# Optimization experiments

Measured on AMD Instinct MI355X. Metric: run time of the kernel, lower is better.

The kernel has to match this reference:

```python
import jax, jax.numpy as jnp
import numpy as np

L = 5          # num_layers
N = 50000      # nodes
E = 600000     # edges
D = 128        # num_features == hidden_units
G = 256        # graphs in batch
O = 10         # num_outputs
BN_EPS = 1e-5


def setup_inputs() -> dict:
    key = jax.random.key(0)
    ks = jax.random.split(key, 8)
    x = jax.random.normal(ks[0], (N, D), jnp.float32)
    edge_index = jax.random.randint(ks[1], (2, E), 0, N, jnp.int32)
    edge_attr = jax.random.randint(ks[2], (E, 3), 0, 8, jnp.int32)
    batch = jnp.sort(jax.random.randint(ks[3], (N,), 0, G, jnp.int32))
    s = 0.05
    return {
        "x": x,
        "edge_index": edge_index,
        "edge_attr": edge_attr,
        "batch": batch,
        "bond_emb": jax.random.normal(ks[4], (L, 3, 8, D), jnp.float32) * s,
        "conv_w1": jax.random.normal(ks[5], (L, D, D), jnp.float32) * s,
        "conv_b1": jnp.zeros((L, D), jnp.float32),
        "conv_bn_gamma": jnp.ones((L, D), jnp.float32),
        "conv_bn_beta": jnp.zeros((L, D), jnp.float32),
        "conv_bn_mean": jnp.zeros((L, D), jnp.float32),
        "conv_bn_var": jnp.ones((L, D), jnp.float32),
        "conv_w2": jax.random.normal(ks[6], (L, D, D), jnp.float32) * s,
        "conv_b2": jnp.zeros((L, D), jnp.float32),
        "bn_gamma": jnp.ones((L, D), jnp.float32),
        "bn_beta": jnp.zeros((L, D), jnp.float32),
        "bn_mean": jnp.zeros((L, D), jnp.float32),
        "bn_var": jnp.ones((L, D), jnp.float32),
        "fc_w": jax.random.normal(ks[7], (L + 1, D, O), jnp.float32) * s,
        "fc_b": jnp.zeros((L + 1, O), jnp.float32),
    }


def _bn_eval(h, gamma, beta, mean, var):
    return (h - mean) * jax.lax.rsqrt(var + BN_EPS) * gamma + beta


def reference(x, edge_index, edge_attr, batch, bond_emb,
              conv_w1, conv_b1, conv_bn_gamma, conv_bn_beta, conv_bn_mean, conv_bn_var,
              conv_w2, conv_b2, bn_gamma, bn_beta, bn_mean, bn_var, fc_w, fc_b):
    src, dst = edge_index[0], edge_index[1]  # x_j = x[src], aggregate at dst
    feat_ids = jnp.arange(3)
    outs = [x]
    for i in range(L):
        # BondEncoder: sum of per-feature embeddings -> [E, D]
        ea = bond_emb[i][feat_ids, edge_attr].sum(axis=1)
        # GINEConv (eps=0): msg = relu(x_j + edge_attr), scatter-add, nn(x + aggr)
        msg = jax.nn.relu(x[src] + ea)
        aggr = jax.ops.segment_sum(msg, dst, num_segments=N)
        h = x + aggr
        h = h @ conv_w1[i] + conv_b1[i]
        h = jax.nn.relu(_bn_eval(h, conv_bn_gamma[i], conv_bn_beta[i], conv_bn_mean[i], conv_bn_var[i]))
        h = h @ conv_w2[i] + conv_b2[i]
        x = jax.nn.relu(_bn_eval(h, bn_gamma[i], bn_beta[i], bn_mean[i], bn_var[i]))
        outs.append(x)
    # global mean pool per layer output, linear head, sum (dropout = identity in eval)
    counts = jax.ops.segment_sum(jnp.ones((N,), x.dtype), batch, num_segments=G)
    inv = 1.0 / jnp.maximum(counts, 1.0)
    out = jnp.zeros((G, O), x.dtype)
    for i, h in enumerate(outs):
        pooled = jax.ops.segment_sum(h, batch, num_segments=G) * inv[:, None]
        out = out + pooled @ fc_w[i] + fc_b[i]
    return out
```

## Files before the change

kernel.cpp:

```cpp
#include <hip/hip_runtime.h>

#define NN 50000
#define EE 600000
#define DD 128
#define GG 256
#define LL 5
#define OO 10
#define BN_EPS 1e-5f
#define CPAD 513

#define B_CVT   3125
#define B_COMBO 1283
#define B_WT    640
#define B_DEG   2344
#define B_INV   1
#define B_POOL0 391
#define B_PREP  (B_CVT + B_COMBO + B_WT + B_DEG + B_INV + B_POOL0)

typedef __attribute__((ext_vector_type(8))) short short8;
typedef __attribute__((ext_vector_type(16))) float float16;

__device__ __forceinline__ unsigned short f2b(float f) {
    unsigned u = __float_as_uint(f);
    unsigned r = u + 0x7FFFu + ((u >> 16) & 1u);
    return (unsigned short)(r >> 16);
}
__device__ __forceinline__ float blo(unsigned u) { return __uint_as_float(u << 16); }
__device__ __forceinline__ float bhi(unsigned u) { return __uint_as_float(u & 0xFFFF0000u); }

__launch_bounds__(256)
__global__ void prep(const float* __restrict__ x, const int* __restrict__ ei,
                     const int* __restrict__ batch, const float* __restrict__ bond,
                     const float* __restrict__ w1, const float* __restrict__ w2,
                     unsigned* __restrict__ xb4, unsigned short* __restrict__ combo,
                     short* __restrict__ wt, int* __restrict__ deg,
                     float* __restrict__ inv, float* __restrict__ pooled0) {
    const int bid = blockIdx.x, t = threadIdx.x;
    if (bid < B_CVT) {
        int gid = bid * 256 + t;
        const float4* xp = (const float4*)(x + (size_t)gid * 8);
        float4 a = xp[0], b = xp[1];
        uint4 o;
        o.x = (unsigned)f2b(a.x) | ((unsigned)f2b(a.y) << 16);
        o.y = (unsigned)f2b(a.z) | ((unsigned)f2b(a.w) << 16);
        o.z = (unsigned)f2b(b.x) | ((unsigned)f2b(b.y) << 16);
        o.w = (unsigned)f2b(b.z) | ((unsigned)f2b(b.w) << 16);
        ((uint4*)xb4)[gid] = o;
    } else if (bid < B_CVT + B_COMBO) {
        int e = (bid - B_CVT) * 256 + t;
        if (e < LL * CPAD * DD) {
            int l = e / (CPAD * DD), rem = e - l * (CPAD * DD);
            int c = rem / DD, d = rem - c * DD;
            float s;
            if (c == 512) s = -1e30f;
            else {
                const float* b_ = bond + (size_t)l * 3 * 8 * DD;
                s = b_[(c & 7) * DD + d] + b_[(8 + ((c >> 3) & 7)) * DD + d]
                  + b_[(16 + (c >> 6)) * DD + d];
            }
            combo[e] = f2b(s);
        }
    } else if (bid < B_CVT + B_COMBO + B_WT) {
        int idx = (bid - B_CVT - B_COMBO) * 256 + t;
        int mat = idx >> 14, e2 = idx & 16383;
        int c = e2 >> 7, k = e2 & 127;
        const float* W = (mat < 5) ? (w1 + (size_t)mat * DD * DD)
                                   : (w2 + (size_t)(mat - 5) * DD * DD);
        wt[idx] = (short)f2b(W[k * DD + c]);
    } else if (bid < B_CVT + B_COMBO + B_WT + B_DEG) {
        int e = (bid - B_CVT - B_COMBO - B_WT) * 256 + t;
        if (e < EE) atomicAdd(&deg[ei[EE + e]], 1);
    } else if (bid < B_CVT + B_COMBO + B_WT + B_DEG + B_INV) {
        __shared__ int sg[GG + 1];
        int g = t, lo = 0, hi = NN;
        while (lo < hi) { int m = (lo + hi) >> 1; if (batch[m] < g) lo = m + 1; else hi = m; }
        sg[g] = lo;
        if (g == 0) sg[GG] = NN;
        __syncthreads();
        inv[g] = 1.0f / fmaxf((float)(sg[g + 1] - sg[g]), 1.0f);
    } else {
        int b = bid - (B_CVT + B_COMBO + B_WT + B_DEG + B_INV);
        int n0 = b * 128;
        __shared__ int sb[128];
        __shared__ float part[4][DD];
        if (t < 128) { int row = n0 + t; sb[t] = (row < NN) ? batch[row] : -1; }
        ((float*)part)[t] = 0.f;
        ((float*)part)[t + 256] = 0.f;
        __syncthreads();
        int gmin = sb[0];
        int col = t & 127, rh = t >> 7;
        float pg[4] = {0.f, 0.f, 0.f, 0.f};
        for (int r = rh; r < 128; r += 2) {
            int s = sb[r];
            float v = (s >= 0) ? x[(size_t)(n0 + r) * DD + col] : 0.f;
            int dg = s - gmin;
#pragma unroll
            for (int j = 0; j < 4; ++j) pg[j] += (dg == j) ? v : 0.f;
        }
#pragma unroll
        for (int j = 0; j < 4; ++j)
            if (pg[j] != 0.f) atomicAdd(&part[j][col], pg[j]);
        __syncthreads();
        for (int q = t; q < 4 * DD; q += 256) {
            int j = q >> 7, c2 = q & 127;
            float v = part[j][c2];
            if (v != 0.f && gmin + j < GG) atomicAdd(&pooled0[(gmin + j) * DD + c2], v);
        }
    }
}

__launch_bounds__(256)
__global__ void alloc_csr(const int* __restrict__ deg, int* __restrict__ cnt,
                          int* __restrict__ off, int* __restrict__ pend,
                          int* __restrict__ epos, unsigned* __restrict__ e_info) {
    int n = blockIdx.x * 256 + threadIdx.x;
    if (n >= NN) return;
    int d = deg[n];
    int pd = (d + 7) & ~7;
    int base = atomicAdd(cnt, pd);
    off[n] = base; epos[n] = base; pend[n] = base + pd;
    for (int i = base + d; i < base + pd; ++i) e_info[i] = (512u << 16);
}

__launch_bounds__(256)
__global__ void scatter_edges(const int* __restrict__ ei, const int* __restrict__ eattr,
                              int* __restrict__ epos, unsigned* __restrict__ e_info) {
    int e = blockIdx.x * 256 + threadIdx.x;
    if (e >= EE) return;
    int dst = ei[EE + e];
    int pos = atomicAdd(&epos[dst], 1);
    unsigned cidx = (unsigned)eattr[e * 3 + 0] | ((unsigned)eattr[e * 3 + 1] << 3)
                  | ((unsigned)eattr[e * 3 + 2] << 6);
    e_info[pos] = (unsigned)ei[e] | (cidx << 16);
}

__launch_bounds__(256)
__global__ void aggr_csr(const unsigned short* __restrict__ xb, const int* __restrict__ off,
                         const int* __restrict__ pend, const unsigned* __restrict__ e_info,
                         const unsigned short* __restrict__ combo,
                         unsigned short* __restrict__ hin) {
    int node = blockIdx.x * 4 + (threadIdx.x >> 6);
    int lane = threadIdx.x & 63;
    if (node >= NN) return;
    int p = off[node], pe = pend[node];
    int d = lane * 2;
    unsigned self = *(const unsigned*)&xb[(size_t)node * DD + d];
    float ax = blo(self), ay = bhi(self);
    for (; p < pe; p += 8) {
        unsigned infv[8], xr[8], cr[8];
#pragma unroll
        for (int j = 0; j < 8; ++j) infv[j] = e_info[p + j];
#pragma unroll
        for (int j = 0; j < 8; ++j) {
            xr[j] = *(const unsigned*)&xb[(size_t)(infv[j] & 0xFFFFu) * DD + d];
            cr[j] = *(const unsigned*)&combo[(size_t)(infv[j] >> 16) * DD + d];
        }
#pragma unroll
        for (int j = 0; j < 8; ++j) {
            ax += fmaxf(blo(xr[j]) + blo(cr[j]), 0.f);
            ay += fmaxf(bhi(xr[j]) + bhi(cr[j]), 0.f);
        }
    }
    *(unsigned*)&hin[(size_t)node * DD + d] = (unsigned)f2b(ax) | ((unsigned)f2b(ay) << 16);
}

__launch_bounds__(256)
__global__ void conv_fused(const unsigned short* __restrict__ hin,
                           const short* __restrict__ Wt1, const short* __restrict__ Wt2,
                           const float* __restrict__ b1, const float* __restrict__ g1,
                           const float* __restrict__ be1, const float* __restrict__ m1,
                           const float* __restrict__ v1,
                           const float* __restrict__ b2, const float* __restrict__ g2,
                           const float* __restrict__ be2, const float* __restrict__ m2,
                           const float* __restrict__ v2,
                           const int* __restrict__ batch,
                           unsigned short* __restrict__ outb,
                           float* __restrict__ pool_slot) {
    __shared__ short As[64 * 136];
    __shared__ int sbg[64];
    const int tid  = threadIdx.x;
    const int lane = tid & 63;
    const int wave = tid >> 6;
    const int row0 = blockIdx.x * 64;

    const int col   = wave * 32 + (lane & 31);
    const int khalf = (lane >> 5) * 8;
    const int arow  = lane & 31;
    const int rbase = 4 * (lane >> 5);
    const int gmin  = batch[row0];

    short8 bf[8];
#pragma unroll
    for (int ch = 0; ch < 8; ++ch)
        bf[ch] = *(const short8*)&Wt1[col * DD + ch * 16 + khalf];

    const float sc1 = g1[col] * rsqrtf(v1[col] + BN_EPS);
    const float sh1 = fmaf(b1[col] - m1[col], sc1, be1[col]);
    const float sc2 = g2[col] * rsqrtf(v2[col] + BN_EPS);
    const float sh2 = fmaf(b2[col] - m2[col], sc2, be2[col]);

    if (tid < 64) {
        int row = row0 + tid;
        sbg[tid] = (row < NN) ? batch[row] - gmin : -1;
    }
    for (int i = tid; i < 1024; i += 256) {
        int r = i >> 4, c8 = (i & 15) * 8;
        int row = row0 + r;
        uint4 z = make_uint4(0, 0, 0, 0);
        if (row < NN) z = *(const uint4*)&hin[(size_t)row * DD + c8];
        *(uint4*)&As[r * 136 + c8] = z;
    }
    __syncthreads();

    float16 acc0 = {0.f,0.f,0.f,0.f,0.f,0.f,0.f,0.f,0.f,0.f,0.f,0.f,0.f,0.f,0.f,0.f};
    float16 acc1 = acc0;
#pragma unroll
    for (int ch = 0; ch < 8; ++ch) {
        short8 a0 = *(const short8*)&As[(arow     ) * 136 + ch * 16 + khalf];
        short8 a1 = *(const short8*)&As[(32 + arow) * 136 + ch * 16 + khalf];
        acc0 = __builtin_amdgcn_mfma_f32_32x32x16_bf16(a0, bf[ch], acc0, 0, 0, 0);
        acc1 = __builtin_amdgcn_mfma_f32_32x32x16_bf16(a1, bf[ch], acc1, 0, 0, 0);
    }

#pragma unroll
    for (int ch = 0; ch < 8; ++ch)
        bf[ch] = *(const short8*)&Wt2[col * DD + ch * 16 + khalf];

    __syncthreads();
#pragma unroll
    for (int r = 0; r < 16; ++r) {
        int rl = (r & 3) + 8 * (r >> 2) + rbase;
        As[rl * 136 + col]        = (short)f2b(fmaxf(fmaf(acc0[r], sc1, sh1), 0.f));
        As[(32 + rl) * 136 + col] = (short)f2b(fmaxf(fmaf(acc1[r], sc1, sh1), 0.f));
    }
    __syncthreads();

    acc0 = acc1 = float16{0.f,0.f,0.f,0.f,0.f,0.f,0.f,0.f,0.f,0.f,0.f,0.f,0.f,0.f,0.f,0.f};
#pragma unroll
    for (int ch = 0; ch < 8; ++ch) {
        short8 a0 = *(const short8*)&As[(arow     ) * 136 + ch * 16 + khalf];
        short8 a1 = *(const short8*)&As[(32 + arow) * 136 + ch * 16 + khalf];
        acc0 = __builtin_amdgcn_mfma_f32_32x32x16_bf16(a0, bf[ch], acc0, 0, 0, 0);
        acc1 = __builtin_amdgcn_mfma_f32_32x32x16_bf16(a1, bf[ch], acc1, 0, 0, 0);
    }

    float pg0 = 0.f, pg1 = 0.f, pg2 = 0.f, pg3 = 0.f;
#pragma unroll
    for (int r = 0; r < 16; ++r) {
        int rl  = (r & 3) + 8 * (r >> 2) + rbase;
        int row = row0 + rl;
        float v0 = fmaxf(fmaf(acc0[r], sc2, sh2), 0.f);
        float v1_ = fmaxf(fmaf(acc1[r], sc2, sh2), 0.f);
        if (row < NN)      outb[(size_t)row * DD + col]        = f2b(v0);
        if (row + 32 < NN) outb[(size_t)(row + 32) * DD + col] = f2b(v1_);
        int ga = sbg[rl], gb = sbg[rl + 32];
        pg0 += ((ga == 0) ? v0 : 0.f) + ((gb == 0) ? v1_ : 0.f);
        pg1 += ((ga == 1) ? v0 : 0.f) + ((gb == 1) ? v1_ : 0.f);
        pg2 += ((ga == 2) ? v0 : 0.f) + ((gb == 2) ? v1_ : 0.f);
        pg3 += ((ga == 3) ? v0 : 0.f) + ((gb == 3) ? v1_ : 0.f);
    }
    pg0 += __shfl_down(pg0, 32);
    pg1 += __shfl_down(pg1, 32);
    pg2 += __shfl_down(pg2, 32);
    pg3 += __shfl_down(pg3, 32);
    if (lane < 32) {
        if (pg0 != 0.f)                 atomicAdd(&pool_slot[(gmin    ) * DD + col], pg0);
        if (pg1 != 0.f && gmin + 1 < GG) atomicAdd(&pool_slot[(gmin + 1) * DD + col], pg1);
        if (pg2 != 0.f && gmin + 2 < GG) atomicAdd(&pool_slot[(gmin + 2) * DD + col], pg2);
        if (pg3 != 0.f && gmin + 3 < GG) atomicAdd(&pool_slot[(gmin + 3) * DD + col], pg3);
    }
}

__launch_bounds__(64)
__global__ void head(const float* __restrict__ pooled, const float* __restrict__ inv,
                     const float* __restrict__ fcw, const float* __restrict__ fcb,
                     float* __restrict__ out) {
    int g = blockIdx.x, t = threadIdx.x;
    __shared__ float part[LL + 1][OO];
    if (t < (LL + 1) * OO) {
        int l = t / OO, o2 = t - l * OO;
        const float* p = pooled + ((size_t)l * GG + g) * DD;
        const float* w = fcw + (size_t)l * DD * OO + o2;
        float s = 0.f;
        for (int d2 = 0; d2 < DD; ++d2) s = fmaf(p[d2], w[(size_t)d2 * OO], s);
        part[l][o2] = s;
    }
    __syncthreads();
    if (t < OO) {
        float sp = 0.f, sb2 = 0.f;
#pragma unroll
        for (int l = 0; l < LL + 1; ++l) { sp += part[l][t]; sb2 += fcb[l * OO + t]; }
        out[g * OO + t] = sp * inv[g] + sb2;
    }
}

extern "C" void kernel_launch(void* const* d_in, const int* in_sizes, int n_in,
                              void* d_out, int out_size, void* d_ws, size_t ws_size,
                              hipStream_t stream) {
    const float* x_in    = (const float*)d_in[0];
    const int*   ei      = (const int*)d_in[1];
    const int*   eattr   = (const int*)d_in[2];
    const int*   batch   = (const int*)d_in[3];
    const float* bond    = (const float*)d_in[4];
    const float* conv_w1 = (const float*)d_in[5];
    const float* conv_b1 = (const float*)d_in[6];
    const float* cbg     = (const float*)d_in[7];
    const float* cbb     = (const float*)d_in[8];
    const float* cbm     = (const float*)d_in[9];
    const float* cbv     = (const float*)d_in[10];
    const float* conv_w2 = (const float*)d_in[11];
    const float* conv_b2 = (const float*)d_in[12];
    const float* bg      = (const float*)d_in[13];
    const float* bb      = (const float*)d_in[14];
    const float* bm      = (const float*)d_in[15];
    const float* bv      = (const float*)d_in[16];
    const float* fcw     = (const float*)d_in[17];
    const float* fcb     = (const float*)d_in[18];
    float* out = (float*)d_out;

    char* base = (char*)d_ws;
    size_t o = 0;
    auto carve = [&](size_t bytes) { void* p = base + o; o += (bytes + 15) & ~(size_t)15; return p; };
    unsigned short* xb     = (unsigned short*)carve((size_t)NN * DD * 2);
    unsigned short* hin    = (unsigned short*)carve((size_t)NN * DD * 2);
    unsigned short* combo  = (unsigned short*)carve((size_t)LL * CPAD * DD * 2);
    short*          wt     = (short*)carve((size_t)10 * DD * DD * 2);
    float*          inv    = (float*)carve(GG * 4);
    int*            off    = (int*)carve(NN * 4);
    int*            pend   = (int*)carve(NN * 4);
    int*            epos   = (int*)carve(NN * 4);
    unsigned*       e_info = (unsigned*)carve(((size_t)EE + 7 * NN) * 4);
    const size_t ZBYTES = (size_t)NN * 4 + 16 + (size_t)(LL + 1) * GG * DD * 4;
    int*   deg    = (int*)carve(ZBYTES);
    int*   cnt    = (int*)((char*)deg + (size_t)NN * 4);
    float* pooled = (float*)((char*)cnt + 16);

    hipMemsetAsync(deg, 0, ZBYTES, stream);

    prep<<<B_PREP, 256, 0, stream>>>(x_in, ei, batch, bond, conv_w1, conv_w2,
                                     (unsigned*)xb, combo, wt, deg, inv, pooled);
    alloc_csr<<<(NN + 255) / 256, 256, 0, stream>>>(deg, cnt, off, pend, epos, e_info);
    scatter_edges<<<(EE + 255) / 256, 256, 0, stream>>>(ei, eattr, epos, e_info);

    const int conv_blocks = (NN + 63) / 64;
    const int aggr_blocks = (NN + 3) / 4;
    for (int i = 0; i < LL; ++i) {
        aggr_csr<<<aggr_blocks, 256, 0, stream>>>(
            xb, off, pend, e_info, combo + (size_t)i * CPAD * DD, hin);
        conv_fused<<<conv_blocks, 256, 0, stream>>>(
            hin, wt + (size_t)i * DD * DD, wt + (size_t)(5 + i) * DD * DD,
            conv_b1 + (size_t)i * DD, cbg + (size_t)i * DD, cbb + (size_t)i * DD,
            cbm + (size_t)i * DD, cbv + (size_t)i * DD,
            conv_b2 + (size_t)i * DD, bg + (size_t)i * DD, bb + (size_t)i * DD,
            bm + (size_t)i * DD, bv + (size_t)i * DD,
            batch, xb, pooled + (size_t)(i + 1) * GG * DD);
    }
    head<<<GG, 64, 0, stream>>>(pooled, inv, fcw, fcb, out);
}
```

Baseline: 456.6 us.

## Fuse edge aggregation into the per-layer MLP kernel with ping-pong buffers

Result: slower. 491.2 us (+7.6%).

```diff
diff --git a/kernel.cpp b/kernel.cpp
--- a/kernel.cpp
+++ b/kernel.cpp
@@ -135,47 +135,20 @@
 }
 
 __launch_bounds__(256)
-__global__ void aggr_csr(const unsigned short* __restrict__ xb, const int* __restrict__ off,
-                         const int* __restrict__ pend, const unsigned* __restrict__ e_info,
-                         const unsigned short* __restrict__ combo,
-                         unsigned short* __restrict__ hin) {
-    int node = blockIdx.x * 4 + (threadIdx.x >> 6);
-    int lane = threadIdx.x & 63;
-    if (node >= NN) return;
-    int p = off[node], pe = pend[node];
-    int d = lane * 2;
-    unsigned self = *(const unsigned*)&xb[(size_t)node * DD + d];
-    float ax = blo(self), ay = bhi(self);
-    for (; p < pe; p += 8) {
-        unsigned infv[8], xr[8], cr[8];
-#pragma unroll
-        for (int j = 0; j < 8; ++j) infv[j] = e_info[p + j];
-#pragma unroll
-        for (int j = 0; j < 8; ++j) {
-            xr[j] = *(const unsigned*)&xb[(size_t)(infv[j] & 0xFFFFu) * DD + d];
-            cr[j] = *(const unsigned*)&combo[(size_t)(infv[j] >> 16) * DD + d];
-        }
-#pragma unroll
-        for (int j = 0; j < 8; ++j) {
-            ax += fmaxf(blo(xr[j]) + blo(cr[j]), 0.f);
-            ay += fmaxf(bhi(xr[j]) + bhi(cr[j]), 0.f);
-        }
-    }
-    *(unsigned*)&hin[(size_t)node * DD + d] = (unsigned)f2b(ax) | ((unsigned)f2b(ay) << 16);
-}
-
-__launch_bounds__(256)
-__global__ void conv_fused(const unsigned short* __restrict__ hin,
-                           const short* __restrict__ Wt1, const short* __restrict__ Wt2,
-                           const float* __restrict__ b1, const float* __restrict__ g1,
-                           const float* __restrict__ be1, const float* __restrict__ m1,
-                           const float* __restrict__ v1,
-                           const float* __restrict__ b2, const float* __restrict__ g2,
-                           const float* __restrict__ be2, const float* __restrict__ m2,
-                           const float* __restrict__ v2,
-                           const int* __restrict__ batch,
-                           unsigned short* __restrict__ outb,
-                           float* __restrict__ pool_slot) {
+__global__ void layer_fused(const unsigned short* __restrict__ xin,
+                            const int* __restrict__ off, const int* __restrict__ pend,
+                            const unsigned* __restrict__ e_info,
+                            const unsigned short* __restrict__ combo,
+                            const short* __restrict__ Wt1, const short* __restrict__ Wt2,
+                            const float* __restrict__ b1, const float* __restrict__ g1,
+                            const float* __restrict__ be1, const float* __restrict__ m1,
+                            const float* __restrict__ v1,
+                            const float* __restrict__ b2, const float* __restrict__ g2,
+                            const float* __restrict__ be2, const float* __restrict__ m2,
+                            const float* __restrict__ v2,
+                            const int* __restrict__ batch,
+                            unsigned short* __restrict__ xout,
+                            float* __restrict__ pool_slot) {
     __shared__ short As[64 * 136];
     __shared__ int sbg[64];
     const int tid  = threadIdx.x;
@@ -203,12 +176,33 @@
         int row = row0 + tid;
         sbg[tid] = (row < NN) ? batch[row] - gmin : -1;
     }
-    for (int i = tid; i < 1024; i += 256) {
-        int r = i >> 4, c8 = (i & 15) * 8;
-        int row = row0 + r;
-        uint4 z = make_uint4(0, 0, 0, 0);
-        if (row < NN) z = *(const uint4*)&hin[(size_t)row * DD + c8];
-        *(uint4*)&As[r * 136 + c8] = z;
+
+    const int d = lane * 2;
+    for (int i = 0; i < 16; ++i) {
+        int rl = wave * 16 + i;
+        int node = row0 + rl;
+        float ax = 0.f, ay = 0.f;
+        if (node < NN) {
+            unsigned self = *(const unsigned*)&xin[(size_t)node * DD + d];
+            ax = blo(self); ay = bhi(self);
+            int p = off[node], pe = pend[node];
+            for (; p < pe; p += 8) {
+                unsigned infv[8], xr[8], cr[8];
+#pragma unroll
+                for (int j = 0; j < 8; ++j) infv[j] = e_info[p + j];
+#pragma unroll
+                for (int j = 0; j < 8; ++j) {
+                    xr[j] = *(const unsigned*)&xin[(size_t)(infv[j] & 0xFFFFu) * DD + d];
+                    cr[j] = *(const unsigned*)&combo[(size_t)(infv[j] >> 16) * DD + d];
+                }
+#pragma unroll
+                for (int j = 0; j < 8; ++j) {
+                    ax += fmaxf(blo(xr[j]) + blo(cr[j]), 0.f);
+                    ay += fmaxf(bhi(xr[j]) + bhi(cr[j]), 0.f);
+                }
+            }
+        }
+        *(unsigned*)&As[rl * 136 + d] = (unsigned)f2b(ax) | ((unsigned)f2b(ay) << 16);
     }
     __syncthreads();
 
@@ -251,8 +245,8 @@
         int row = row0 + rl;
         float v0 = fmaxf(fmaf(acc0[r], sc2, sh2), 0.f);
         float v1_ = fmaxf(fmaf(acc1[r], sc2, sh2), 0.f);
-        if (row < NN)      outb[(size_t)row * DD + col]        = f2b(v0);
-        if (row + 32 < NN) outb[(size_t)(row + 32) * DD + col] = f2b(v1_);
+        if (row < NN)      xout[(size_t)row * DD + col]        = f2b(v0);
+        if (row + 32 < NN) xout[(size_t)(row + 32) * DD + col] = f2b(v1_);
         int ga = sbg[rl], gb = sbg[rl + 32];
         pg0 += ((ga == 0) ? v0 : 0.f) + ((gb == 0) ? v1_ : 0.f);
         pg1 += ((ga == 1) ? v0 : 0.f) + ((gb == 1) ? v1_ : 0.f);
@@ -264,7 +258,7 @@
     pg2 += __shfl_down(pg2, 32);
     pg3 += __shfl_down(pg3, 32);
     if (lane < 32) {
-        if (pg0 != 0.f)                 atomicAdd(&pool_slot[(gmin    ) * DD + col], pg0);
+        if (pg0 != 0.f)                  atomicAdd(&pool_slot[(gmin    ) * DD + col], pg0);
         if (pg1 != 0.f && gmin + 1 < GG) atomicAdd(&pool_slot[(gmin + 1) * DD + col], pg1);
         if (pg2 != 0.f && gmin + 2 < GG) atomicAdd(&pool_slot[(gmin + 2) * DD + col], pg2);
         if (pg3 != 0.f && gmin + 3 < GG) atomicAdd(&pool_slot[(gmin + 3) * DD + col], pg3);
@@ -321,8 +315,8 @@
     char* base = (char*)d_ws;
     size_t o = 0;
     auto carve = [&](size_t bytes) { void* p = base + o; o += (bytes + 15) & ~(size_t)15; return p; };
-    unsigned short* xb     = (unsigned short*)carve((size_t)NN * DD * 2);
-    unsigned short* hin    = (unsigned short*)carve((size_t)NN * DD * 2);
+    unsigned short* xbA    = (unsigned short*)carve((size_t)NN * DD * 2);
+    unsigned short* xbB    = (unsigned short*)carve((size_t)NN * DD * 2);
     unsigned short* combo  = (unsigned short*)carve((size_t)LL * CPAD * DD * 2);
     short*          wt     = (short*)carve((size_t)10 * DD * DD * 2);
     float*          inv    = (float*)carve(GG * 4);
@@ -338,22 +332,23 @@
     hipMemsetAsync(deg, 0, ZBYTES, stream);
 
     prep<<<B_PREP, 256, 0, stream>>>(x_in, ei, batch, bond, conv_w1, conv_w2,
-                                     (unsigned*)xb, combo, wt, deg, inv, pooled);
+                                     (unsigned*)xbA, combo, wt, deg, inv, pooled);
     alloc_csr<<<(NN + 255) / 256, 256, 0, stream>>>(deg, cnt, off, pend, epos, e_info);
     scatter_edges<<<(EE + 255) / 256, 256, 0, stream>>>(ei, eattr, epos, e_info);
 
     const int conv_blocks = (NN + 63) / 64;
-    const int aggr_blocks = (NN + 3) / 4;
+    unsigned short* xin  = xbA;
+    unsigned short* xout = xbB;
     for (int i = 0; i < LL; ++i) {
-        aggr_csr<<<aggr_blocks, 256, 0, stream>>>(
-            xb, off, pend, e_info, combo + (size_t)i * CPAD * DD, hin);
-        conv_fused<<<conv_blocks, 256, 0, stream>>>(
-            hin, wt + (size_t)i * DD * DD, wt + (size_t)(5 + i) * DD * DD,
+        layer_fused<<<conv_blocks, 256, 0, stream>>>(
+            xin, off, pend, e_info, combo + (size_t)i * CPAD * DD,
+            wt + (size_t)i * DD * DD, wt + (size_t)(5 + i) * DD * DD,
             conv_b1 + (size_t)i * DD, cbg + (size_t)i * DD, cbb + (size_t)i * DD,
             cbm + (size_t)i * DD, cbv + (size_t)i * DD,
             conv_b2 + (size_t)i * DD, bg + (size_t)i * DD, bb + (size_t)i * DD,
             bm + (size_t)i * DD, bv + (size_t)i * DD,
-            batch, xb, pooled + (size_t)(i + 1) * GG * DD);
+            batch, xout, pooled + (size_t)(i + 1) * GG * DD);
+        unsigned short* tmp = xin; xin = xout; xout = tmp;
     }
     head<<<GG, 64, 0, stream>>>(pooled, inv, fcw, fcb, out);
 }
```

## Use fixed-stride ELL edge layout and vectorize neighbor aggregation

Applied to the files above, without the earlier changes.

After: 431.3 us. -5.5%, faster.

```diff
diff --git a/kernel.cpp b/kernel.cpp
--- a/kernel.cpp
+++ b/kernel.cpp
@@ -8,14 +8,17 @@
 #define OO 10
 #define BN_EPS 1e-5f
 #define CPAD 513
+#define ESTRIDE 40
+#define SENT (512u << 16)
 
 #define B_CVT   3125
 #define B_COMBO 1283
-#define B_WT    640
-#define B_DEG   2344
+#define B_WT    160
+#define B_EFILL 1954
+#define B_EPOS  196
 #define B_INV   1
 #define B_POOL0 391
-#define B_PREP  (B_CVT + B_COMBO + B_WT + B_DEG + B_INV + B_POOL0)
+#define B_PREP  (B_CVT + B_COMBO + B_WT + B_EFILL + B_EPOS + B_INV + B_POOL0)
 
 typedef __attribute__((ext_vector_type(8))) short short8;
 typedef __attribute__((ext_vector_type(16))) float float16;
@@ -25,26 +28,28 @@
     unsigned r = u + 0x7FFFu + ((u >> 16) & 1u);
     return (unsigned short)(r >> 16);
 }
+__device__ __forceinline__ unsigned pk2(float lo, float hi) {
+    return (unsigned)f2b(lo) | ((unsigned)f2b(hi) << 16);
+}
 __device__ __forceinline__ float blo(unsigned u) { return __uint_as_float(u << 16); }
 __device__ __forceinline__ float bhi(unsigned u) { return __uint_as_float(u & 0xFFFF0000u); }
 
 __launch_bounds__(256)
-__global__ void prep(const float* __restrict__ x, const int* __restrict__ ei,
-                     const int* __restrict__ batch, const float* __restrict__ bond,
+__global__ void prep(const float* __restrict__ x, const int* __restrict__ batch,
+                     const float* __restrict__ bond,
                      const float* __restrict__ w1, const float* __restrict__ w2,
                      unsigned* __restrict__ xb4, unsigned short* __restrict__ combo,
-                     short* __restrict__ wt, int* __restrict__ deg,
-                     float* __restrict__ inv, float* __restrict__ pooled0) {
+                     short* __restrict__ wt, unsigned* __restrict__ e_info,
+                     int* __restrict__ epos, float* __restrict__ inv,
+                     float* __restrict__ pooled0) {
     const int bid = blockIdx.x, t = threadIdx.x;
     if (bid < B_CVT) {
         int gid = bid * 256 + t;
         const float4* xp = (const float4*)(x + (size_t)gid * 8);
         float4 a = xp[0], b = xp[1];
         uint4 o;
-        o.x = (unsigned)f2b(a.x) | ((unsigned)f2b(a.y) << 16);
-        o.y = (unsigned)f2b(a.z) | ((unsigned)f2b(a.w) << 16);
-        o.z = (unsigned)f2b(b.x) | ((unsigned)f2b(b.y) << 16);
-        o.w = (unsigned)f2b(b.z) | ((unsigned)f2b(b.w) << 16);
+        o.x = pk2(a.x, a.y); o.y = pk2(a.z, a.w);
+        o.z = pk2(b.x, b.y); o.w = pk2(b.z, b.w);
         ((uint4*)xb4)[gid] = o;
     } else if (bid < B_CVT + B_COMBO) {
         int e = (bid - B_CVT) * 256 + t;
@@ -61,16 +66,32 @@
             combo[e] = f2b(s);
         }
     } else if (bid < B_CVT + B_COMBO + B_WT) {
-        int idx = (bid - B_CVT - B_COMBO) * 256 + t;
-        int mat = idx >> 14, e2 = idx & 16383;
-        int c = e2 >> 7, k = e2 & 127;
+        __shared__ float tile[32][33];
+        int b = bid - B_CVT - B_COMBO;
+        int mat = b >> 4, tl = b & 15;
+        int k0 = (tl >> 2) * 32, c0 = (tl & 3) * 32;
         const float* W = (mat < 5) ? (w1 + (size_t)mat * DD * DD)
                                    : (w2 + (size_t)(mat - 5) * DD * DD);
-        wt[idx] = (short)f2b(W[k * DD + c]);
-    } else if (bid < B_CVT + B_COMBO + B_WT + B_DEG) {
-        int e = (bid - B_CVT - B_COMBO - B_WT) * 256 + t;
-        if (e < EE) atomicAdd(&deg[ei[EE + e]], 1);
-    } else if (bid < B_CVT + B_COMBO + B_WT + B_DEG + B_INV) {
+        int j = t & 31, q = t >> 5;
+#pragma unroll
+        for (int rr = 0; rr < 4; ++rr) {
+            int row = q + rr * 8;
+            tile[row][j] = W[(size_t)(k0 + row) * DD + c0 + j];
+        }
+        __syncthreads();
+#pragma unroll
+        for (int rr = 0; rr < 4; ++rr) {
+            int cr = q + rr * 8;
+            wt[(size_t)mat * DD * DD + (size_t)(c0 + cr) * DD + k0 + j] = (short)f2b(tile[j][cr]);
+        }
+    } else if (bid < B_CVT + B_COMBO + B_WT + B_EFILL) {
+        int gid = (bid - B_CVT - B_COMBO - B_WT) * 256 + t;
+        if (gid < NN * ESTRIDE / 4)
+            ((uint4*)e_info)[gid] = make_uint4(SENT, SENT, SENT, SENT);
+    } else if (bid < B_CVT + B_COMBO + B_WT + B_EFILL + B_EPOS) {
+        int n = (bid - B_CVT - B_COMBO - B_WT - B_EFILL) * 256 + t;
+        if (n < NN) epos[n] = n * ESTRIDE;
+    } else if (bid < B_CVT + B_COMBO + B_WT + B_EFILL + B_EPOS + B_INV) {
         __shared__ int sg[GG + 1];
         int g = t, lo = 0, hi = NN;
         while (lo < hi) { int m = (lo + hi) >> 1; if (batch[m] < g) lo = m + 1; else hi = m; }
@@ -79,7 +100,7 @@
         __syncthreads();
         inv[g] = 1.0f / fmaxf((float)(sg[g + 1] - sg[g]), 1.0f);
     } else {
-        int b = bid - (B_CVT + B_COMBO + B_WT + B_DEG + B_INV);
+        int b = bid - (B_CVT + B_COMBO + B_WT + B_EFILL + B_EPOS + B_INV);
         int n0 = b * 128;
         __shared__ int sb[128];
         __shared__ float part[4][DD];
@@ -95,31 +116,18 @@
             float v = (s >= 0) ? x[(size_t)(n0 + r) * DD + col] : 0.f;
             int dg = s - gmin;
 #pragma unroll
-            for (int j = 0; j < 4; ++j) pg[j] += (dg == j) ? v : 0.f;
-        }
-#pragma unroll
-        for (int j = 0; j < 4; ++j)
-            if (pg[j] != 0.f) atomicAdd(&part[j][col], pg[j]);
+            for (int jj = 0; jj < 4; ++jj) pg[jj] += (dg == jj) ? v : 0.f;
+        }
+#pragma unroll
+        for (int jj = 0; jj < 4; ++jj)
+            if (pg[jj] != 0.f) atomicAdd(&part[jj][col], pg[jj]);
         __syncthreads();
-        for (int q = t; q < 4 * DD; q += 256) {
-            int j = q >> 7, c2 = q & 127;
-            float v = part[j][c2];
-            if (v != 0.f && gmin + j < GG) atomicAdd(&pooled0[(gmin + j) * DD + c2], v);
-        }
-    }
-}
-
-__launch_bounds__(256)
-__global__ void alloc_csr(const int* __restrict__ deg, int* __restrict__ cnt,
-                          int* __restrict__ off, int* __restrict__ pend,
-                          int* __restrict__ epos, unsigned* __restrict__ e_info) {
-    int n = blockIdx.x * 256 + threadIdx.x;
-    if (n >= NN) return;
-    int d = deg[n];
-    int pd = (d + 7) & ~7;
-    int base = atomicAdd(cnt, pd);
-    off[n] = base; epos[n] = base; pend[n] = base + pd;
-    for (int i = base + d; i < base + pd; ++i) e_info[i] = (512u << 16);
+        for (int q2 = t; q2 < 4 * DD; q2 += 256) {
+            int jj = q2 >> 7, c2 = q2 & 127;
+            float v = part[jj][c2];
+            if (v != 0.f && gmin + jj < GG) atomicAdd(&pooled0[(gmin + jj) * DD + c2], v);
+        }
+    }
 }
 
 __launch_bounds__(256)
@@ -135,33 +143,53 @@
 }
 
 __launch_bounds__(256)
-__global__ void aggr_csr(const unsigned short* __restrict__ xb, const int* __restrict__ off,
-                         const int* __restrict__ pend, const unsigned* __restrict__ e_info,
+__global__ void aggr_csr(const unsigned short* __restrict__ xin,
+                         const int* __restrict__ epos,
+                         const unsigned* __restrict__ e_info,
                          const unsigned short* __restrict__ combo,
                          unsigned short* __restrict__ hin) {
     int node = blockIdx.x * 4 + (threadIdx.x >> 6);
     int lane = threadIdx.x & 63;
     if (node >= NN) return;
-    int p = off[node], pe = pend[node];
-    int d = lane * 2;
-    unsigned self = *(const unsigned*)&xb[(size_t)node * DD + d];
-    float ax = blo(self), ay = bhi(self);
-    for (; p < pe; p += 8) {
-        unsigned infv[8], xr[8], cr[8];
-#pragma unroll
-        for (int j = 0; j < 8; ++j) infv[j] = e_info[p + j];
-#pragma unroll
-        for (int j = 0; j < 8; ++j) {
-            xr[j] = *(const unsigned*)&xb[(size_t)(infv[j] & 0xFFFFu) * DD + d];
-            cr[j] = *(const unsigned*)&combo[(size_t)(infv[j] >> 16) * DD + d];
-        }
-#pragma unroll
-        for (int j = 0; j < 8; ++j) {
-            ax += fmaxf(blo(xr[j]) + blo(cr[j]), 0.f);
-            ay += fmaxf(bhi(xr[j]) + bhi(cr[j]), 0.f);
-        }
-    }
-    *(unsigned*)&hin[(size_t)node * DD + d] = (unsigned)f2b(ax) | ((unsigned)f2b(ay) << 16);
+    const int base = node * ESTRIDE;
+    const int deg  = epos[node] - base;
+    const int pe   = base + ((deg + 7) & ~7);
+    const int eg   = lane >> 4;
+    const int f    = (lane & 15) * 8;
+    float acc[8];
+#pragma unroll
+    for (int i = 0; i < 8; ++i) acc[i] = 0.f;
+
+    for (int p = base; p < pe; p += 8) {
+        unsigned i0 = e_info[p + eg];
+        unsigned i1 = e_info[p + 4 + eg];
+        uint4 xv0 = *(const uint4*)&xin[(size_t)(i0 & 0xFFFFu) * DD + f];
+        uint4 cv0 = *(const uint4*)&combo[(size_t)(i0 >> 16) * DD + f];
+        uint4 xv1 = *(const uint4*)&xin[(size_t)(i1 & 0xFFFFu) * DD + f];
+        uint4 cv1 = *(const uint4*)&combo[(size_t)(i1 >> 16) * DD + f];
+        acc[0] += fmaxf(blo(xv0.x) + blo(cv0.x), 0.f) + fmaxf(blo(xv1.x) + blo(cv1.x), 0.f);
+        acc[1] += fmaxf(bhi(xv0.x) + bhi(cv0.x), 0.f) + fmaxf(bhi(xv1.x) + bhi(cv1.x), 0.f);
+        acc[2] += fmaxf(blo(xv0.y) + blo(cv0.y), 0.f) + fmaxf(blo(xv1.y) + blo(cv1.y), 0.f);
+        acc[3] += fmaxf(bhi(xv0.y) + bhi(cv0.y), 0.f) + fmaxf(bhi(xv1.y) + bhi(cv1.y), 0.f);
+        acc[4] += fmaxf(blo(xv0.z) + blo(cv0.z), 0.f) + fmaxf(blo(xv1.z) + blo(cv1.z), 0.f);
+        acc[5] += fmaxf(bhi(xv0.z) + bhi(cv0.z), 0.f) + fmaxf(bhi(xv1.z) + bhi(cv1.z), 0.f);
+        acc[6] += fmaxf(blo(xv0.w) + blo(cv0.w), 0.f) + fmaxf(blo(xv1.w) + blo(cv1.w), 0.f);
+        acc[7] += fmaxf(bhi(xv0.w) + bhi(cv0.w), 0.f) + fmaxf(bhi(xv1.w) + bhi(cv1.w), 0.f);
+    }
+#pragma unroll
+    for (int i = 0; i < 8; ++i) {
+        acc[i] += __shfl_xor(acc[i], 16, 64);
+        acc[i] += __shfl_xor(acc[i], 32, 64);
+    }
+    if (lane < 16) {
+        uint4 self = *(const uint4*)&xin[(size_t)node * DD + f];
+        uint4 o;
+        o.x = pk2(acc[0] + blo(self.x), acc[1] + bhi(self.x));
+        o.y = pk2(acc[2] + blo(self.y), acc[3] + bhi(self.y));
+        o.z = pk2(acc[4] + blo(self.z), acc[5] + bhi(self.z));
+        o.w = pk2(acc[6] + blo(self.w), acc[7] + bhi(self.w));
+        *(uint4*)&hin[(size_t)node * DD + f] = o;
+    }
 }
 
 __launch_bounds__(256)
@@ -264,7 +292,7 @@
     pg2 += __shfl_down(pg2, 32);
     pg3 += __shfl_down(pg3, 32);
     if (lane < 32) {
-        if (pg0 != 0.f)                 atomicAdd(&pool_slot[(gmin    ) * DD + col], pg0);
+        if (pg0 != 0.f)                  atomicAdd(&pool_slot[(gmin    ) * DD + col], pg0);
         if (pg1 != 0.f && gmin + 1 < GG) atomicAdd(&pool_slot[(gmin + 1) * DD + col], pg1);
         if (pg2 != 0.f && gmin + 2 < GG) atomicAdd(&pool_slot[(gmin + 2) * DD + col], pg2);
         if (pg3 != 0.f && gmin + 3 < GG) atomicAdd(&pool_slot[(gmin + 3) * DD + col], pg3);
@@ -321,39 +349,36 @@
     char* base = (char*)d_ws;
     size_t o = 0;
     auto carve = [&](size_t bytes) { void* p = base + o; o += (bytes + 15) & ~(size_t)15; return p; };
-    unsigned short* xb     = (unsigned short*)carve((size_t)NN * DD * 2);
-    unsigned short* hin    = (unsigned short*)carve((size_t)NN * DD * 2);
+    unsigned short* xbA    = (unsigned short*)carve((size_t)NN * DD * 2);
+    unsigned short* xbB    = (unsigned short*)carve((size_t)NN * DD * 2);
     unsigned short* combo  = (unsigned short*)carve((size_t)LL * CPAD * DD * 2);
     short*          wt     = (short*)carve((size_t)10 * DD * DD * 2);
     float*          inv    = (float*)carve(GG * 4);
-    int*            off    = (int*)carve(NN * 4);
-    int*            pend   = (int*)carve(NN * 4);
     int*            epos   = (int*)carve(NN * 4);
-    unsigned*       e_info = (unsigned*)carve(((size_t)EE + 7 * NN) * 4);
-    const size_t ZBYTES = (size_t)NN * 4 + 16 + (size_t)(LL + 1) * GG * DD * 4;
-    int*   deg    = (int*)carve(ZBYTES);
-    int*   cnt    = (int*)((char*)deg + (size_t)NN * 4);
-    float* pooled = (float*)((char*)cnt + 16);
-
-    hipMemsetAsync(deg, 0, ZBYTES, stream);
-
-    prep<<<B_PREP, 256, 0, stream>>>(x_in, ei, batch, bond, conv_w1, conv_w2,
-                                     (unsigned*)xb, combo, wt, deg, inv, pooled);
-    alloc_csr<<<(NN + 255) / 256, 256, 0, stream>>>(deg, cnt, off, pend, epos, e_info);
+    unsigned*       e_info = (unsigned*)carve((size_t)NN * ESTRIDE * 4);
+    float*          pooled = (float*)carve((size_t)(LL + 1) * GG * DD * 4);
+
+    hipMemsetAsync(pooled, 0, (size_t)(LL + 1) * GG * DD * 4, stream);
+
+    prep<<<B_PREP, 256, 0, stream>>>(x_in, batch, bond, conv_w1, conv_w2,
+                                     (unsigned*)xbA, combo, wt, e_info, epos, inv, pooled);
     scatter_edges<<<(EE + 255) / 256, 256, 0, stream>>>(ei, eattr, epos, e_info);
 
     const int conv_blocks = (NN + 63) / 64;
     const int aggr_blocks = (NN + 3) / 4;
+    unsigned short* xin  = xbA;
+    unsigned short* xout = xbB;
     for (int i = 0; i < LL; ++i) {
         aggr_csr<<<aggr_blocks, 256, 0, stream>>>(
-            xb, off, pend, e_info, combo + (size_t)i * CPAD * DD, hin);
+            xin, epos, e_info, combo + (size_t)i * CPAD * DD, xout );
         conv_fused<<<conv_blocks, 256, 0, stream>>>(
-            hin, wt + (size_t)i * DD * DD, wt + (size_t)(5 + i) * DD * DD,
+            xout , wt + (size_t)i * DD * DD, wt + (size_t)(5 + i) * DD * DD,
             conv_b1 + (size_t)i * DD, cbg + (size_t)i * DD, cbb + (size_t)i * DD,
             cbm + (size_t)i * DD, cbv + (size_t)i * DD,
             conv_b2 + (size_t)i * DD, bg + (size_t)i * DD, bb + (size_t)i * DD,
             bm + (size_t)i * DD, bv + (size_t)i * DD,
-            batch, xb, pooled + (size_t)(i + 1) * GG * DD);
+            batch, xin ,
+            pooled + (size_t)(i + 1) * GG * DD);
     }
     head<<<GG, 64, 0, stream>>>(pooled, inv, fcw, fcb, out);
 }
```
